# Optimization experiments

Measured on AMD Instinct MI355X. Metric: run time of the kernel, lower is better.

## Reference

```python
import jax, jax.numpy as jnp
import numpy as np

DIM = 768
NUM_HEADS = 12
HEAD_DIM = DIM // NUM_HEADS
WS = 14                       # window_size (14, 14)
N_TOK = WS * WS + 1           # 197 (patches + cls)
NUM_REL = (2 * WS - 1) ** 2 + 3  # 732
SCALE = HEAD_DIM ** -0.5


def _build_rel_index():
    # Faithful port of the BEiT relative_position_index construction.
    coords = np.stack(np.meshgrid(np.arange(WS), np.arange(WS), indexing='ij'))  # (2, WS, WS)
    flat = coords.reshape(2, -1)                                   # (2, WS*WS)
    rel = flat[:, :, None] - flat[:, None, :]                      # (2, P, P)
    rel = rel.transpose(1, 2, 0).astype(np.int64)                  # (P, P, 2)
    rel[:, :, 0] += WS - 1
    rel[:, :, 1] += WS - 1
    rel[:, :, 0] *= 2 * WS - 1
    idx = np.zeros((N_TOK, N_TOK), dtype=np.int64)
    idx[1:, 1:] = rel.sum(-1)
    idx[0, :] = NUM_REL - 3
    idx[:, 0] = NUM_REL - 2
    idx[0, 0] = NUM_REL - 1
    return idx


def setup_inputs() -> dict:
    key = jax.random.key(0)
    ks = jax.random.split(key, 7)
    B = 64
    x = jax.random.normal(ks[0], (B, N_TOK, DIM), dtype=jnp.float32)
    qkv_w = jax.random.normal(ks[1], (3 * DIM, DIM), dtype=jnp.float32) * 0.02
    q_bias = jnp.zeros((DIM,), dtype=jnp.float32)
    v_bias = jnp.zeros((DIM,), dtype=jnp.float32)
    rel_table = jax.random.normal(ks[2], (NUM_REL, NUM_HEADS), dtype=jnp.float32) * 0.02
    proj_w = jax.random.normal(ks[3], (DIM, DIM), dtype=jnp.float32) * 0.02
    proj_b = jnp.zeros((DIM,), dtype=jnp.float32)
    rel_index = jnp.asarray(_build_rel_index())  # (N, N) int64
    return {"x": x, "qkv_w": qkv_w, "q_bias": q_bias, "v_bias": v_bias,
            "rel_table": rel_table, "proj_w": proj_w, "proj_b": proj_b,
            "rel_index": rel_index}


def reference(x, qkv_w, q_bias, v_bias, rel_table, proj_w, proj_b, rel_index):
    B, N, C = x.shape
    # qkv bias = concat(q_bias, zeros, v_bias)
    qkv_b = jnp.concatenate([q_bias, jnp.zeros_like(v_bias), v_bias])
    qkv = x @ qkv_w.T + qkv_b                       # (B, N, 3C)
    qkv = qkv.reshape(B, N, 3, NUM_HEADS, HEAD_DIM).transpose(2, 0, 3, 1, 4)
    q, k, v = qkv[0], qkv[1], qkv[2]                # each (B, H, N, hd)
    attn = jnp.einsum('bhqd,bhkd->bhqk', q * SCALE, k)
    # relative position bias gathered from table: (N, N, H) -> (H, N, N)
    bias = rel_table[rel_index].transpose(2, 0, 1)
    attn = attn + bias[None]
    attn = jax.nn.softmax(attn, axis=-1)
    out = jnp.einsum('bhqk,bhkd->bhqd', attn, v)    # (B, H, N, hd)
    out = out.transpose(0, 2, 1, 3).reshape(B, N, -1)
    return out @ proj_w.T + proj_b
```

## Files before the change

kernel.cpp:

```cpp
#include <hip/hip_runtime.h>
#include <stdint.h>

#define NTOK 197
#define HD 64
#define NH 12
#define CDIM 768
#define BB 64
#define MTOT (BB*NTOK)
#define MPAD 12672
#define SCALE 0.125f

typedef __attribute__((ext_vector_type(8))) short short8;
typedef __attribute__((ext_vector_type(4))) float f32x4;
typedef unsigned short us;

__device__ __forceinline__ us f2b(float f){
    union { float f; uint32_t u; } v; v.f = f;
    uint32_t u = v.u;
    uint32_t r = u + 0x7fffu + ((u >> 16) & 1u);
    return (us)(r >> 16);
}

__device__ __forceinline__ float b2f(us b){
    union { uint32_t u; float f; } v; v.u = ((uint32_t)b) << 16;
    return v.f;
}

__device__ __forceinline__ void gload16(const us* g, us* l){
    __builtin_amdgcn_global_load_lds((const __attribute__((address_space(1))) void*)g,
                                     (__attribute__((address_space(3))) void*)l, 16, 0, 0);
}

__global__ void cvt_kernel(const float* __restrict__ in, us* __restrict__ out, int n4){
    int i = blockIdx.x*blockDim.x + threadIdx.x;
    if (i < n4){
        float4 v = ((const float4*)in)[i];
        ushort4 o;
        o.x = f2b(v.x); o.y = f2b(v.y); o.z = f2b(v.z); o.w = f2b(v.w);
        ((ushort4*)out)[i] = o;
    }
}

__global__ void bias_kernel(const int* __restrict__ rel_index, const float* __restrict__ rel_table,
                            float* __restrict__ biasm){
    int i = blockIdx.x*blockDim.x + threadIdx.x;
    if (i < NTOK*NTOK){
        int idx = rel_index[i];
        #pragma unroll
        for (int h = 0; h < NH; ++h)
            biasm[h*NTOK*NTOK + i] = rel_table[idx*NH + h];
    }
}

__global__ __launch_bounds__(512,1) void pgemm2_kernel(
    const us* __restrict__ A, const us* __restrict__ Bw,
    us* __restrict__ Qo, us* __restrict__ Ko, us* __restrict__ Vo,
    const float* __restrict__ b0, const float* __restrict__ b2, int ny, int total)
{
    __shared__ __align__(16) us AsB[2][24576];
    __shared__ __align__(16) us cbuf[128*132];
    const int tid  = threadIdx.x;
    const int lane = tid & 63;
    const int wave = tid >> 6;
    const int wrr = wave >> 2;
    const int wcc = wave & 3;
    const int lr = lane & 15;
    const int g  = lane >> 4;

    const int id  = blockIdx.x;
    const int xcd = id & 7;
    const int j   = id >> 3;
    const int qs  = total >> 3, rs = total & 7;
    const int S   = xcd*qs + (xcd < rs ? xcd : rs);
    const int L   = qs + (xcd < rs ? 1 : 0);
    const int qb  = L >> 5, rb = L & 31;
    const int cnt = qb + (j < rb ? 1 : 0);
    const int w0  = S + j*qb + (j < rb ? j : rb);
    if (cnt == 0) return;

    int aoff[2], bofs[4];
    int aldo[2], bldo[4];
    #pragma unroll
    for (int p=0;p<2;p++){
        int c = tid + p*512;
        int row = c >> 3, ch = c & 7;
        aoff[p] = row*CDIM + ((ch ^ (row & 7))*8);
        aldo[p] = c*8;
    }
    #pragma unroll
    for (int jj=0;jj<4;jj++){
        int c = tid + jj*512;
        int row = c >> 3, ch = c & 7;
        bofs[jj] = row*CDIM + ((ch ^ (row & 7))*8);
        bldo[jj] = 8192 + c*8;
    }

    auto stage = [&](int buf, const us* pA, const us* pB, int kt){
        #pragma unroll
        for (int p=0;p<2;p++) gload16(pA + aoff[p] + kt*64, &AsB[buf][aldo[p]]);
        #pragma unroll
        for (int jj=0;jj<4;jj++) gload16(pB + bofs[jj] + kt*64, &AsB[buf][bldo[jj]]);
    };

    int w  = w0;
    int bx = w / ny, by = w - bx*ny;
    int m0 = bx*128, n0 = by*256;
    const us* pA = A  + (size_t)m0*CDIM;
    const us* pB = Bw + (size_t)n0*CDIM;
    stage(0, pA, pB, 0);
    int buf = 0;

    #pragma unroll 1
    for (int tt = 0; tt < cnt; ++tt){
        int w1 = w + 1;
        int bx1 = w1 / ny, by1 = w1 - bx1*ny;
        const us* pA1 = A  + (size_t)(bx1*128)*CDIM;
        const us* pB1 = Bw + (size_t)(by1*256)*CDIM;

        const int whc = n0 / CDIM;
        float addf[4];
        const float sclf = (whc == 0) ? SCALE : 1.f;
        #pragma unroll
        for (int nt=0;nt<4;nt++){
            int n = n0 + wcc*64 + nt*16 + lr;
            int hn = n - whc*CDIM;
            addf[nt] = (whc == 0) ? b0[hn] : (whc == 2 ? b2[hn] : 0.f);
        }

        f32x4 acc[4][4];
        #pragma unroll
        for (int i=0;i<4;i++)
            #pragma unroll
            for (int jj=0;jj<4;jj++) acc[i][jj] = (f32x4){0.f,0.f,0.f,0.f};

        #pragma unroll 1
        for (int kt = 0; kt < 12; ++kt){
            asm volatile("s_waitcnt vmcnt(0)" ::: "memory");
            __builtin_amdgcn_s_barrier();
            if (kt < 11)           stage(buf^1, pA,  pB,  kt+1);
            else if (tt+1 < cnt)   stage(buf^1, pA1, pB1, 0);
            const us* la = &AsB[buf][0];
            const us* lb = &AsB[buf][8192];
            #pragma unroll
            for (int kk=0; kk<2; ++kk){
                const int co = 8*((kk*4 + g) ^ (lr & 7));
                short8 af[4], bf[4];
                #pragma unroll
                for (int mt=0;mt<4;mt++)
                    af[mt] = *(const short8*)&la[(wrr*64+mt*16+lr)*64 + co];
                #pragma unroll
                for (int nt=0;nt<4;nt++)
                    bf[nt] = *(const short8*)&lb[(wcc*64+nt*16+lr)*64 + co];
                __builtin_amdgcn_s_setprio(1);
                #pragma unroll
                for (int mt=0;mt<4;mt++)
                    #pragma unroll
                    for (int nt=0;nt<4;nt++)
                        acc[mt][nt] = __builtin_amdgcn_mfma_f32_16x16x32_bf16(af[mt], bf[nt], acc[mt][nt], 0,0,0);
                __builtin_amdgcn_s_setprio(0);
            }
            buf ^= 1;
        }

        const us* outp = (whc == 0 ? Qo : (whc == 1 ? Ko : Vo));
        #pragma unroll 1
        for (int half = 0; half < 2; ++half){
            if ((wcc >> 1) == half){
                #pragma unroll
                for (int mt=0;mt<4;mt++)
                    #pragma unroll
                    for (int rr=0;rr<4;rr++){
                        int row = wrr*64 + mt*16 + g*4 + rr;
                        #pragma unroll
                        for (int nt=0;nt<4;nt++){
                            int col = (wcc & 1)*64 + nt*16 + lr;
                            cbuf[row*132 + col] = f2b((acc[mt][nt][rr] + addf[nt]) * sclf);
                        }
                    }
            }
            __syncthreads();
            #pragma unroll
            for (int p=0;p<4;p++){
                int c = tid + p*512;
                int row = c >> 4, ch = c & 15;
                int m = m0 + row;
                if (m < MTOT){
                    short8 vv = *(const short8*)&cbuf[row*132 + ch*8];
                    int n = n0 + half*128 + ch*8;
                    int hn = n - whc*CDIM;
                    int h  = hn >> 6, d0 = hn & 63;
                    int bidx = m / NTOK;
                    int tok  = m - bidx*NTOK;
                    size_t off = ((size_t)((bidx*NH + h)*NTOK + tok))*HD + d0;
                    *(short8*)((us*)outp + off) = vv;
                }
            }
            __syncthreads();
        }

        w = w1; m0 = bx1*128; n0 = by1*256; pA = pA1; pB = pB1;
    }
}

__global__ __launch_bounds__(256) void proj_gemm_kernel(
    const us* __restrict__ A, const us* __restrict__ Bw,
    float* __restrict__ Cout, const float* __restrict__ b0, int ny)
{
    __shared__ __align__(16) us lds[32768];
    us* As = lds;
    us* Bs = lds + 16384;
    const int tid  = threadIdx.x;
    const int lane = tid & 63;
    const int wave = tid >> 6;
    const int wr = wave >> 1, wc = wave & 1;
    const int lr = lane & 15;
    const int g  = lane >> 4;

    const int NB   = gridDim.x;
    const int base = NB >> 3;
    const int rem  = NB & 7;
    const int id   = blockIdx.x;
    const int xcd  = id & 7;
    const int qq   = id >> 3;
    const int start = (xcd < rem) ? xcd*(base+1) : rem*(base+1) + (xcd-rem)*base;
    const int w    = start + qq;
    const int bx   = w / ny;
    const int by   = w - bx*ny;
    const int m0 = bx * 128;
    const int n0 = by * 128;
    const int NT = CDIM / 128;

    const int row0 = tid >> 4;
    const int cg   = (tid & 15) ^ row0;

    float addf[4];
    #pragma unroll
    for (int nt=0;nt<4;nt++) addf[nt] = b0[n0 + wc*64 + nt*16 + lr];

    f32x4 acc[4][4];
    #pragma unroll
    for (int i=0;i<4;i++)
        #pragma unroll
        for (int j=0;j<4;j++) acc[i][j] = (f32x4){0.f,0.f,0.f,0.f};

    const us* gA = A  + (size_t)(m0 + row0)*CDIM + cg*8;
    const us* gB = Bw + (size_t)(n0 + row0)*CDIM + cg*8;

    #pragma unroll 1
    for (int kt = 0; kt < NT; ++kt){
        __syncthreads();
        #pragma unroll
        for (int j=0;j<8;j++){
            gload16(gA + (size_t)j*16*CDIM + kt*128, As + tid*8 + j*2048);
            gload16(gB + (size_t)j*16*CDIM + kt*128, Bs + tid*8 + j*2048);
        }
        __syncthreads();
        #pragma unroll
        for (int kk=0; kk<4; ++kk){
            const int co = 8*((kk*4 + g) ^ lr);
            short8 af[4], bf[4];
            #pragma unroll
            for (int mt=0;mt<4;mt++)
                af[mt] = *(const short8*)&As[(wr*64+mt*16+lr)*128 + co];
            #pragma unroll
            for (int nt=0;nt<4;nt++)
                bf[nt] = *(const short8*)&Bs[(wc*64+nt*16+lr)*128 + co];
            __builtin_amdgcn_s_setprio(1);
            #pragma unroll
            for (int mt=0;mt<4;mt++)
                #pragma unroll
                for (int nt=0;nt<4;nt++)
                    acc[mt][nt] = __builtin_amdgcn_mfma_f32_16x16x32_bf16(af[mt], bf[nt], acc[mt][nt], 0,0,0);
            __builtin_amdgcn_s_setprio(0);
        }
    }

    __syncthreads();
    #pragma unroll
    for (int mt=0;mt<4;mt++)
        #pragma unroll
        for (int r=0;r<4;r++){
            int row = wr*64 + mt*16 + g*4 + r;
            #pragma unroll
            for (int nt=0;nt<4;nt++){
                int col = wc*64 + nt*16 + lr;
                lds[row*132 + col] = f2b(acc[mt][nt][r] + addf[nt]);
            }
        }
    __syncthreads();
    #pragma unroll
    for (int j=0;j<8;j++){
        int c2  = tid + j*256;
        int row = c2 >> 4;
        int ch  = c2 & 15;
        int m = m0 + row;
        if (m >= MTOT) continue;
        short8 vv = *(const short8*)&lds[row*132 + ch*8];
        int n = n0 + ch*8;
        float4 f0, f1;
        f0.x = b2f((us)vv[0]); f0.y = b2f((us)vv[1]); f0.z = b2f((us)vv[2]); f0.w = b2f((us)vv[3]);
        f1.x = b2f((us)vv[4]); f1.y = b2f((us)vv[5]); f1.z = b2f((us)vv[6]); f1.w = b2f((us)vv[7]);
        *(float4*)&Cout[(size_t)m*CDIM + n]     = f0;
        *(float4*)&Cout[(size_t)m*CDIM + n + 4] = f1;
    }
}

__global__ __launch_bounds__(256) void attn_kernel(
    const us* __restrict__ Q,
    const us* __restrict__ K,
    const us* __restrict__ V,
    const float* __restrict__ biasm,
    us* __restrict__ Ao)
{
    __shared__ us Vt[64][232];
    __shared__ us Ps[4][16][232];
    const int bh = blockIdx.x;
    const int b = bh / NH;
    const int h = bh - b*NH;
    const us* Qh = Q + (size_t)bh*NTOK*HD;
    const us* Kh = K + (size_t)bh*NTOK*HD;
    const us* Vh = V + (size_t)bh*NTOK*HD;
    const float* bh_bias = biasm + (size_t)h*NTOK*NTOK;
    const int tid = threadIdx.x, lane = tid & 63, wave = tid >> 6;
    const int lr = lane & 15, g = lane >> 4, ko = g*8;

    for (int i = tid; i < 64*232/2; i += 256) ((uint32_t*)Vt)[i] = 0;
    __syncthreads();
    {
        int d0 = (tid & 7) * 8;
        for (int t = tid >> 3; t < NTOK; t += 32){
            short8 v = *(const short8*)&Vh[t*HD + d0];
            #pragma unroll
            for (int j=0;j<8;j++) Vt[d0+j][t] = (us)v[j];
        }
    }
    __syncthreads();

    for (int s = wave; s < 13; s += 4){
        int qrow = s*16 + lr; qrow = qrow > 196 ? 196 : qrow;
        short8 qa0 = *(const short8*)&Qh[qrow*HD + ko];
        short8 qa1 = *(const short8*)&Qh[qrow*HD + 32 + ko];
        f32x4 S[13];
        #pragma unroll
        for (int t=0;t<13;t++){
            int kc = t*16 + lr; kc = kc > 196 ? 196 : kc;
            short8 kb0 = *(const short8*)&Kh[kc*HD + ko];
            short8 kb1 = *(const short8*)&Kh[kc*HD + 32 + ko];
            f32x4 a = (f32x4){0.f,0.f,0.f,0.f};
            a = __builtin_amdgcn_mfma_f32_16x16x32_bf16(qa0, kb0, a, 0,0,0);
            a = __builtin_amdgcn_mfma_f32_16x16x32_bf16(qa1, kb1, a, 0,0,0);
            S[t] = a;
        }
        float rmax[4] = {-3e38f,-3e38f,-3e38f,-3e38f};
        #pragma unroll
        for (int t=0;t<13;t++){
            int col = t*16 + lr;
            bool cok = col < NTOK;
            int colc = cok ? col : 196;
            #pragma unroll
            for (int r=0;r<4;r++){
                int row = s*16 + g*4 + r; row = row > 196 ? 196 : row;
                float xv = S[t][r] + bh_bias[row*NTOK + colc];
                xv = cok ? xv : -1e30f;
                S[t][r] = xv;
                rmax[r] = fmaxf(rmax[r], xv);
            }
        }
        #pragma unroll
        for (int r=0;r<4;r++)
            #pragma unroll
            for (int msk=1; msk<16; msk<<=1)
                rmax[r] = fmaxf(rmax[r], __shfl_xor(rmax[r], msk));
        float rsum[4] = {0.f,0.f,0.f,0.f};
        #pragma unroll
        for (int t=0;t<13;t++)
            #pragma unroll
            for (int r=0;r<4;r++){
                float e = __expf(S[t][r] - rmax[r]);
                S[t][r] = e;
                rsum[r] += e;
            }
        #pragma unroll
        for (int r=0;r<4;r++){
            #pragma unroll
            for (int msk=1; msk<16; msk<<=1)
                rsum[r] += __shfl_xor(rsum[r], msk);
            rsum[r] = 1.f / rsum[r];
        }
        #pragma unroll
        for (int t=0;t<13;t++)
            #pragma unroll
            for (int r=0;r<4;r++)
                Ps[wave][g*4+r][t*16+lr] = f2b(S[t][r] * rsum[r]);
        #pragma unroll
        for (int r=0;r<4;r++) Ps[wave][g*4+r][208+lr] = 0;
        asm volatile("s_waitcnt lgkmcnt(0)" ::: "memory");
        f32x4 pv[4];
        #pragma unroll
        for (int nt=0;nt<4;nt++) pv[nt] = (f32x4){0.f,0.f,0.f,0.f};
        #pragma unroll
        for (int ks=0; ks<7; ks++){
            int k0 = ks*32 + ko;
            short8 pa = *(const short8*)&Ps[wave][lr][k0];
            #pragma unroll
            for (int nt=0;nt<4;nt++){
                short8 vb = *(const short8*)&Vt[nt*16+lr][k0];
                pv[nt] = __builtin_amdgcn_mfma_f32_16x16x32_bf16(pa, vb, pv[nt], 0,0,0);
            }
        }
        #pragma unroll
        for (int nt=0;nt<4;nt++)
            #pragma unroll
            for (int r=0;r<4;r++){
                int tok = s*16 + g*4 + r;
                if (tok < NTOK)
                    Ao[(size_t)(b*NTOK + tok)*CDIM + h*HD + nt*16 + lr] = f2b(pv[nt][r]);
            }
    }
}

extern "C" void kernel_launch(void* const* d_in, const int* in_sizes, int n_in,
                              void* d_out, int out_size, void* d_ws, size_t ws_size,
                              hipStream_t stream)
{
    const float* x        = (const float*)d_in[0];
    const float* qkv_w    = (const float*)d_in[1];
    const float* q_bias   = (const float*)d_in[2];
    const float* v_bias   = (const float*)d_in[3];
    const float* rel_tab  = (const float*)d_in[4];
    const float* proj_w   = (const float*)d_in[5];
    const float* proj_b   = (const float*)d_in[6];
    const int*   rel_idx  = (const int*)d_in[7];
    float* out = (float*)d_out;

    char* w = (char*)d_ws;
    us* xb    = (us*)w; w += (size_t)MPAD*CDIM*2;
    us* wqkv  = (us*)w; w += (size_t)3*CDIM*CDIM*2;
    us* wproj = (us*)w; w += (size_t)CDIM*CDIM*2;
    us* Qb    = (us*)w; w += (size_t)BB*NH*NTOK*HD*2;
    us* Kb    = (us*)w; w += (size_t)BB*NH*NTOK*HD*2;
    us* Vb    = (us*)w; w += (size_t)BB*NH*NTOK*HD*2;
    float* biasm = (float*)w; w += (size_t)NH*NTOK*NTOK*4;
    us* aob   = (us*)w; w += (size_t)MPAD*CDIM*2;

    int n1 = MTOT*CDIM/4;
    cvt_kernel<<<(n1+255)/256, 256, 0, stream>>>(x, xb, n1);
    int n2 = 3*CDIM*CDIM/4;
    cvt_kernel<<<(n2+255)/256, 256, 0, stream>>>(qkv_w, wqkv, n2);
    int n3 = CDIM*CDIM/4;
    cvt_kernel<<<(n3+255)/256, 256, 0, stream>>>(proj_w, wproj, n3);
    bias_kernel<<<(NTOK*NTOK+255)/256, 256, 0, stream>>>(rel_idx, rel_tab, biasm);

    pgemm2_kernel<<<256, 512, 0, stream>>>(xb, wqkv, Qb, Kb, Vb, q_bias, v_bias, 9, 891);
    attn_kernel<<<BB*NH, 256, 0, stream>>>(Qb, Kb, Vb, biasm, aob);
    proj_gemm_kernel<<<594, 256, 0, stream>>>(aob, wproj, out, proj_b, 6);
}
```

Measured before the change: 177.6 us.

## Pipeline QKV GEMM loads two k-steps ahead with partial vmcnt waits

Reworks the QKV projection GEMM's global-to-LDS pipeline so loads are issued two steps ahead across a flattened k-step sequence that spans tile boundaries. Each step waits only for the older batch of loads (vmcnt(6)) instead of draining all outstanding loads. The refill for a buffer is issued after an LDS-read barrier at the end of the step, so the next tile's prefetch continues through the epilogue. This is meant to hide global memory latency behind MFMA work, at the cost of an extra barrier per k-step and more address arithmetic per stage.

```diff
diff --git a/kernel.cpp b/kernel.cpp
--- a/kernel.cpp
+++ b/kernel.cpp
@@ -31,6 +31,9 @@
                                      (__attribute__((address_space(3))) void*)l, 16, 0, 0);
 }
 
+#define LGKM0_BAR() do{ asm volatile("s_waitcnt lgkmcnt(0)" ::: "memory"); \
+                        __builtin_amdgcn_s_barrier(); }while(0)
+
 __global__ void cvt_kernel(const float* __restrict__ in, us* __restrict__ out, int n4){
     int i = blockIdx.x*blockDim.x + threadIdx.x;
     if (i < n4){
@@ -52,7 +55,7 @@
     }
 }
 
-__global__ __launch_bounds__(512,1) void pgemm2_kernel(
+__global__ __launch_bounds__(512,1) void pgemm3_kernel(
     const us* __restrict__ A, const us* __restrict__ Bw,
     us* __restrict__ Qo, us* __restrict__ Ko, us* __restrict__ Vo,
     const float* __restrict__ b0, const float* __restrict__ b2, int ny, int total)
@@ -69,13 +72,13 @@
 
     const int id  = blockIdx.x;
     const int xcd = id & 7;
-    const int j   = id >> 3;
+    const int jb  = id >> 3;
     const int qs  = total >> 3, rs = total & 7;
-    const int S   = xcd*qs + (xcd < rs ? xcd : rs);
+    const int Ssp = xcd*qs + (xcd < rs ? xcd : rs);
     const int L   = qs + (xcd < rs ? 1 : 0);
     const int qb  = L >> 5, rb = L & 31;
-    const int cnt = qb + (j < rb ? 1 : 0);
-    const int w0  = S + j*qb + (j < rb ? j : rb);
+    const int cnt = qb + (jb < rb ? 1 : 0);
+    const int w0  = Ssp + jb*qb + (jb < rb ? jb : rb);
     if (cnt == 0) return;
 
     int aoff[2], bofs[4];
@@ -95,28 +98,29 @@
         bldo[jj] = 8192 + c*8;
     }
 
-    auto stage = [&](int buf, const us* pA, const us* pB, int kt){
+    const int S = cnt * 12;
+    auto stageStep = [&](int x){
+        int tt = x / 12, kt = x - tt*12;
+        int ww = w0 + tt;
+        int bx = ww / ny, by = ww - bx*ny;
+        const us* pA = A  + (size_t)(bx*128)*CDIM;
+        const us* pB = Bw + (size_t)(by*256)*CDIM;
+        int buf = x & 1;
         #pragma unroll
         for (int p=0;p<2;p++) gload16(pA + aoff[p] + kt*64, &AsB[buf][aldo[p]]);
         #pragma unroll
         for (int jj=0;jj<4;jj++) gload16(pB + bofs[jj] + kt*64, &AsB[buf][bldo[jj]]);
     };
 
-    int w  = w0;
-    int bx = w / ny, by = w - bx*ny;
-    int m0 = bx*128, n0 = by*256;
-    const us* pA = A  + (size_t)m0*CDIM;
-    const us* pB = Bw + (size_t)n0*CDIM;
-    stage(0, pA, pB, 0);
-    int buf = 0;
+    stageStep(0);
+    if (S > 1) stageStep(1);
+    int s = 0;
 
     #pragma unroll 1
     for (int tt = 0; tt < cnt; ++tt){
-        int w1 = w + 1;
-        int bx1 = w1 / ny, by1 = w1 - bx1*ny;
-        const us* pA1 = A  + (size_t)(bx1*128)*CDIM;
-        const us* pB1 = Bw + (size_t)(by1*256)*CDIM;
-
+        const int w  = w0 + tt;
+        const int bx = w / ny, by = w - bx*ny;
+        const int m0 = bx*128, n0 = by*256;
         const int whc = n0 / CDIM;
         float addf[4];
         const float sclf = (whc == 0) ? SCALE : 1.f;
@@ -135,12 +139,11 @@
 
         #pragma unroll 1
         for (int kt = 0; kt < 12; ++kt){
-            asm volatile("s_waitcnt vmcnt(0)" ::: "memory");
+            if (s == S-1) asm volatile("s_waitcnt vmcnt(0)" ::: "memory");
+            else          asm volatile("s_waitcnt vmcnt(6)" ::: "memory");
             __builtin_amdgcn_s_barrier();
-            if (kt < 11)           stage(buf^1, pA,  pB,  kt+1);
-            else if (tt+1 < cnt)   stage(buf^1, pA1, pB1, 0);
-            const us* la = &AsB[buf][0];
-            const us* lb = &AsB[buf][8192];
+            const us* la = &AsB[s & 1][0];
+            const us* lb = &AsB[s & 1][8192];
             #pragma unroll
             for (int kk=0; kk<2; ++kk){
                 const int co = 8*((kk*4 + g) ^ (lr & 7));
@@ -159,7 +162,9 @@
                         acc[mt][nt] = __builtin_amdgcn_mfma_f32_16x16x32_bf16(af[mt], bf[nt], acc[mt][nt], 0,0,0);
                 __builtin_amdgcn_s_setprio(0);
             }
-            buf ^= 1;
+            LGKM0_BAR();
+            if (s + 2 < S) stageStep(s + 2);
+            ++s;
         }
 
         const us* outp = (whc == 0 ? Qo : (whc == 1 ? Ko : Vo));
@@ -178,7 +183,7 @@
                         }
                     }
             }
-            __syncthreads();
+            LGKM0_BAR();
             #pragma unroll
             for (int p=0;p<4;p++){
                 int c = tid + p*512;
@@ -195,10 +200,8 @@
                     *(short8*)((us*)outp + off) = vv;
                 }
             }
-            __syncthreads();
-        }
-
-        w = w1; m0 = bx1*128; n0 = by1*256; pA = pA1; pB = pB1;
+            LGKM0_BAR();
+        }
     }
 }
 
@@ -451,7 +454,7 @@
     cvt_kernel<<<(n3+255)/256, 256, 0, stream>>>(proj_w, wproj, n3);
     bias_kernel<<<(NTOK*NTOK+255)/256, 256, 0, stream>>>(rel_idx, rel_tab, biasm);
 
-    pgemm2_kernel<<<256, 512, 0, stream>>>(xb, wqkv, Qb, Kb, Vb, q_bias, v_bias, 9, 891);
+    pgemm3_kernel<<<256, 512, 0, stream>>>(xb, wqkv, Qb, Kb, Vb, q_bias, v_bias, 9, 891);
     attn_kernel<<<BB*NH, 256, 0, stream>>>(Qb, Kb, Vb, biasm, aob);
     proj_gemm_kernel<<<594, 256, 0, stream>>>(aob, wproj, out, proj_b, 6);
 }
```

After: 175.3 us. Within noise of the previous version (-1.3%).
